# Kernel optimization log

Hardware: AMD Instinct MI355X
Metric: run time of the kernel (lower is better)

Reference implementation:

```python
import jax, jax.numpy as jnp
import numpy as np

EPS = 1e-5

@jax.custom_vjp
def ste_quantize(w):
    # abs-mean scale, round, clamp to {-1, 0, 1}
    scale = jnp.maximum(jnp.mean(jnp.abs(w)), EPS)
    return jnp.clip(jnp.round(w / scale), -1.0, 1.0)

def _ste_fwd(w):
    return ste_quantize(w), None

def _ste_bwd(_, g):
    # straight-through: gradient passes unchanged
    return (g,)

ste_quantize.defvjp(_ste_fwd, _ste_bwd)


def setup_inputs() -> dict:
    key = jax.random.key(0)
    k1, k2 = jax.random.split(key)
    x = jax.random.normal(k1, (8, 8192, 1024), dtype=jnp.float32)       # [B, S, in]
    weight = jax.random.normal(k2, (1024, 1024), dtype=jnp.float32) * 0.02  # [out, in]
    return {"x": x, "weight": weight}


def reference(x, weight):
    w_ternary = ste_quantize(weight)                         # [out, in] in {-1,0,1}
    scale = jnp.maximum(jnp.mean(jnp.abs(weight)), EPS)      # scalar (differentiable path)
    # F.linear(x, w_ternary * scale): out = x @ (w_ternary*scale)^T
    return jnp.einsum('bsi,oi->bso', x, w_ternary * scale)
```

## Files before the change

### kernel.cpp

```cpp
#include <hip/hip_runtime.h>
#include <stdint.h>

#define K_DIM 1024
#define N_DIM 1024

#define BM 256
#define BN 256
#define BK 32
#define NKT (K_DIM / BK)
#define NBUF 3
#define A_TILE (BM * BK)
#define B_TILE (BN * BK)

typedef __attribute__((ext_vector_type(8))) __bf16 bf16x8;
typedef __attribute__((ext_vector_type(4))) float f32x4;

__device__ __align__(16) unsigned short g_wq[N_DIM * K_DIM];
__device__ double g_partial[256];
__device__ float g_scale;

__device__ __forceinline__ unsigned int pack_bf16(float hi, float lo) {
  return __builtin_amdgcn_perm(__float_as_uint(hi), __float_as_uint(lo), 0x07060302u);
}

__global__ void absum_kernel(const float* __restrict__ w) {
  const int tid = threadIdx.x, bid = blockIdx.x;
  const float4* w4 = (const float4*)w;
  double s = 0.0;
#pragma unroll
  for (int i = 0; i < 4; i++) {
    float4 v = w4[bid * 1024 + i * 256 + tid];
    s += (double)fabsf(v.x) + (double)fabsf(v.y) + (double)fabsf(v.z) + (double)fabsf(v.w);
  }
#pragma unroll
  for (int o = 32; o > 0; o >>= 1) s += __shfl_down(s, o);
  __shared__ double sm[4];
  if ((tid & 63) == 0) sm[tid >> 6] = s;
  __syncthreads();
  if (tid == 0) g_partial[bid] = sm[0] + sm[1] + sm[2] + sm[3];
}

__global__ void scale_kernel() {
  const int tid = threadIdx.x;
  double v = g_partial[tid];
#pragma unroll
  for (int o = 32; o > 0; o >>= 1) v += __shfl_down(v, o);
  __shared__ double sm[4];
  if ((tid & 63) == 0) sm[tid >> 6] = v;
  __syncthreads();
  if (tid == 0) {
    double total = sm[0] + sm[1] + sm[2] + sm[3];
    double mean = total * (1.0 / 1048576.0);
    g_scale = (float)fmax(mean, 1e-5);
  }
}

__global__ void quant_kernel(const float* __restrict__ w) {
  const int idx = blockIdx.x * 256 + threadIdx.x;
  const float s = g_scale;
  float4 v = ((const float4*)w)[idx];
  float q0 = fminf(1.f, fmaxf(-1.f, rintf(v.x / s)));
  float q1 = fminf(1.f, fmaxf(-1.f, rintf(v.y / s)));
  float q2 = fminf(1.f, fmaxf(-1.f, rintf(v.z / s)));
  float q3 = fminf(1.f, fmaxf(-1.f, rintf(v.w / s)));
  ushort4 o;
  o.x = (unsigned short)(__float_as_uint(q0) >> 16);
  o.y = (unsigned short)(__float_as_uint(q1) >> 16);
  o.z = (unsigned short)(__float_as_uint(q2) >> 16);
  o.w = (unsigned short)(__float_as_uint(q3) >> 16);
  ((ushort4*)g_wq)[idx] = o;
}

__global__ __launch_bounds__(512, 2) void bitlinear_gemm(const float* __restrict__ x,
                                                         float* __restrict__ C) {
  __shared__ __align__(16) unsigned short As[NBUF * A_TILE];
  __shared__ __align__(16) unsigned short Bs[NBUF * B_TILE];

  const int tid  = threadIdx.x;
  const int lane = tid & 63;
  const int wave = tid >> 6;
  const int wm   = wave >> 2;
  const int wn   = wave & 3;
  const int lm   = lane & 15;
  const int lq   = lane >> 4;

  const int b       = blockIdx.x;
  const int cpx     = (int)(gridDim.x >> 3);
  const int logical = (b & 7) * cpx + (b >> 3);
  const int mt      = logical >> 2;
  const int nt      = logical & 3;
  const int m0      = mt * BM;
  const int n0      = nt * BN;

  f32x4 acc[8][4];
#pragma unroll
  for (int i = 0; i < 8; i++)
#pragma unroll
    for (int j = 0; j < 4; j++) acc[i][j] = (f32x4){0.f, 0.f, 0.f, 0.f};

  const int cswz = ((lane & 3) ^ ((lane >> 3) & 3)) * 8;
  const unsigned short* bSrc =
      g_wq + (size_t)(n0 + wave * 32 + (lane >> 2)) * K_DIM + cswz;
  const int ldsDst = wave * 32 * BK;

#define STAGE_B(tt, bb)                                                        \
  do {                                                                         \
    const unsigned short* s_ = bSrc + (tt) * BK;                               \
    unsigned short* d_ = &Bs[(bb) * B_TILE + ldsDst];                          \
    __builtin_amdgcn_global_load_lds(                                          \
        (const __attribute__((address_space(1))) unsigned int*)s_,             \
        (__attribute__((address_space(3))) unsigned int*)d_, 16, 0, 0);        \
    __builtin_amdgcn_global_load_lds(                                          \
        (const __attribute__((address_space(1))) unsigned int*)(s_ + 16 * K_DIM), \
        (__attribute__((address_space(3))) unsigned int*)(d_ + 16 * BK), 16, 0, 0); \
  } while (0)

  const int arow = wave * 32 + (lane >> 1);
  const int ah   = lane & 1;
  const int aswz = (lane >> 2) & 3;
  const float4* aGlb =
      (const float4*)(x + (size_t)(m0 + arow) * K_DIM + ah * 16);
  const int wo0 = arow * BK + (((2 * ah) ^ aswz) * 8);
  const int wo1 = arow * BK + (((2 * ah + 1) ^ aswz) * 8);

  float4 aR0, aR1, aR2, aR3;

#define LOAD_A(tt)                                                             \
  do {                                                                         \
    const float4* p_ = aGlb + (tt) * 8;                                        \
    aR0 = p_[0]; aR1 = p_[1]; aR2 = p_[2]; aR3 = p_[3];                        \
  } while (0)

#define CVT_WRITE_A(bb)                                                        \
  do {                                                                         \
    uint4 p0_, p1_;                                                            \
    p0_.x = pack_bf16(aR0.y, aR0.x); p0_.y = pack_bf16(aR0.w, aR0.z);          \
    p0_.z = pack_bf16(aR1.y, aR1.x); p0_.w = pack_bf16(aR1.w, aR1.z);          \
    p1_.x = pack_bf16(aR2.y, aR2.x); p1_.y = pack_bf16(aR2.w, aR2.z);          \
    p1_.z = pack_bf16(aR3.y, aR3.x); p1_.w = pack_bf16(aR3.w, aR3.z);          \
    *(uint4*)&As[(bb) * A_TILE + wo0] = p0_;                                   \
    *(uint4*)&As[(bb) * A_TILE + wo1] = p1_;                                   \
  } while (0)

  const int xorc = (((lm >> 1) & 3) ^ lq) * 8;
  const int aRd  = (wm * 128 + lm) * BK + xorc;
  const int bRd  = (wn * 64 + lm) * BK + xorc;

  {
    float4 t0, t1, t2, t3;
    {
      const float4* p_ = aGlb;
      t0 = p_[0]; t1 = p_[1]; t2 = p_[2]; t3 = p_[3];
    }
    STAGE_B(0, 0);
    LOAD_A(1);
    STAGE_B(1, 1);
    uint4 p0_, p1_;
    p0_.x = pack_bf16(t0.y, t0.x); p0_.y = pack_bf16(t0.w, t0.z);
    p0_.z = pack_bf16(t1.y, t1.x); p0_.w = pack_bf16(t1.w, t1.z);
    p1_.x = pack_bf16(t2.y, t2.x); p1_.y = pack_bf16(t2.w, t2.z);
    p1_.z = pack_bf16(t3.y, t3.x); p1_.w = pack_bf16(t3.w, t3.z);
    *(uint4*)&As[wo0] = p0_;
    *(uint4*)&As[wo1] = p1_;
  }
  asm volatile("s_waitcnt vmcnt(6) lgkmcnt(0)\n\ts_barrier" ::: "memory");

  int buf = 0;
#pragma unroll 1
  for (int t = 0; t < NKT; ++t) {
    const unsigned short* Ab = &As[buf * A_TILE + aRd];
    const unsigned short* Bb = &Bs[buf * B_TILE + bRd];
    const int nbuf = (buf + 2 >= NBUF) ? buf + 2 - NBUF : buf + 2;
    const int wbuf = (buf + 1 == NBUF) ? 0 : buf + 1;

    bf16x8 bfr[4], af[4];
#pragma unroll
    for (int nf = 0; nf < 4; ++nf) bfr[nf] = *(const bf16x8*)(Bb + nf * 16 * BK);
#pragma unroll
    for (int mf = 0; mf < 4; ++mf) af[mf] = *(const bf16x8*)(Ab + mf * 16 * BK);

    __builtin_amdgcn_s_setprio(1);
#pragma unroll
    for (int mf = 0; mf < 4; ++mf)
#pragma unroll
      for (int nf = 0; nf < 4; ++nf)
        acc[mf][nf] = __builtin_amdgcn_mfma_f32_16x16x32_bf16(af[mf], bfr[nf],
                                                              acc[mf][nf], 0, 0, 0);
    __builtin_amdgcn_s_setprio(0);

    bf16x8 af2[4];
#pragma unroll
    for (int mf = 0; mf < 4; ++mf)
      af2[mf] = *(const bf16x8*)(Ab + (mf + 4) * 16 * BK);

    if (t < NKT - 1) CVT_WRITE_A(wbuf);
    if (t < NKT - 2) {
      LOAD_A(t + 2);
      STAGE_B(t + 2, nbuf);
    }

    __builtin_amdgcn_s_setprio(1);
#pragma unroll
    for (int mf = 0; mf < 4; ++mf)
#pragma unroll
      for (int nf = 0; nf < 4; ++nf)
        acc[mf + 4][nf] = __builtin_amdgcn_mfma_f32_16x16x32_bf16(
            af2[mf], bfr[nf], acc[mf + 4][nf], 0, 0, 0);
    __builtin_amdgcn_s_setprio(0);

    if (t < NKT - 2)
      asm volatile("s_waitcnt vmcnt(6) lgkmcnt(0)\n\ts_barrier" ::: "memory");
    else if (t < NKT - 1)
      asm volatile("s_waitcnt vmcnt(0) lgkmcnt(0)\n\ts_barrier" ::: "memory");

    buf = wbuf;
  }
#undef STAGE_B
#undef LOAD_A
#undef CVT_WRITE_A

  const float s    = g_scale;
  const int   crow = m0 + wm * 128 + lq * 4;
  const int   ccol = n0 + wn * 64 + lm;
#pragma unroll
  for (int mf = 0; mf < 8; ++mf) {
#pragma unroll
    for (int nf = 0; nf < 4; ++nf) {
#pragma unroll
      for (int r = 0; r < 4; ++r) {
        C[(size_t)(crow + mf * 16 + r) * N_DIM + (ccol + nf * 16)] =
            acc[mf][nf][r] * s;
      }
    }
  }
}

extern "C" void kernel_launch(void* const* d_in, const int* in_sizes, int n_in,
                              void* d_out, int out_size, void* d_ws, size_t ws_size,
                              hipStream_t stream) {
  const float* x = (const float*)d_in[0];
  const float* w = (const float*)d_in[1];
  float* out = (float*)d_out;
  const int M = in_sizes[0] / K_DIM;

  hipLaunchKernelGGL(absum_kernel, dim3(256), dim3(256), 0, stream, w);
  hipLaunchKernelGGL(scale_kernel, dim3(1), dim3(256), 0, stream);
  hipLaunchKernelGGL(quant_kernel, dim3(1024), dim3(256), 0, stream, w);
  hipLaunchKernelGGL(bitlinear_gemm,
                     dim3((unsigned)(((size_t)M / BM) * (N_DIM / BN))),
                     dim3(512), 0, stream, x, out);
}
```

Before: 565.9 us.

## Shrink GEMM tiles to 128x128 with 4 waves and double buffering

Block tile drops from 256x256 with 8 waves to 128x128 with 4 waves. The triple-buffered, two-half MFMA pipeline becomes a simpler double-buffered loop that stages the next tile before one MFMA batch. The grid grows fourfold and launch bounds target more resident blocks per CU, aiming for better occupancy and latency hiding. In exchange, each x row tile is re-read and converted from fp32 to bf16 twice as often, and each block does fewer MFMAs per LDS byte.

```diff
diff --git a/kernel.cpp b/kernel.cpp
--- a/kernel.cpp
+++ b/kernel.cpp
@@ -4,11 +4,11 @@
 #define K_DIM 1024
 #define N_DIM 1024
 
-#define BM 256
-#define BN 256
+#define BM 128
+#define BN 128
 #define BK 32
 #define NKT (K_DIM / BK)
-#define NBUF 3
+#define NBUF 2
 #define A_TILE (BM * BK)
 #define B_TILE (BN * BK)
 
@@ -71,7 +71,7 @@
   ((ushort4*)g_wq)[idx] = o;
 }
 
-__global__ __launch_bounds__(512, 2) void bitlinear_gemm(const float* __restrict__ x,
+__global__ __launch_bounds__(256, 4) void bitlinear_gemm(const float* __restrict__ x,
                                                          float* __restrict__ C) {
   __shared__ __align__(16) unsigned short As[NBUF * A_TILE];
   __shared__ __align__(16) unsigned short Bs[NBUF * B_TILE];
@@ -79,22 +79,22 @@
   const int tid  = threadIdx.x;
   const int lane = tid & 63;
   const int wave = tid >> 6;
-  const int wm   = wave >> 2;
-  const int wn   = wave & 3;
+  const int wm   = (wave >> 1) * 64;
+  const int wn   = (wave & 1) * 64;
   const int lm   = lane & 15;
   const int lq   = lane >> 4;
 
   const int b       = blockIdx.x;
   const int cpx     = (int)(gridDim.x >> 3);
   const int logical = (b & 7) * cpx + (b >> 3);
-  const int mt      = logical >> 2;
-  const int nt      = logical & 3;
+  const int mt      = logical >> 3;
+  const int nt      = logical & 7;
   const int m0      = mt * BM;
   const int n0      = nt * BN;
 
-  f32x4 acc[8][4];
-#pragma unroll
-  for (int i = 0; i < 8; i++)
+  f32x4 acc[4][4];
+#pragma unroll
+  for (int i = 0; i < 4; i++)
 #pragma unroll
     for (int j = 0; j < 4; j++) acc[i][j] = (f32x4){0.f, 0.f, 0.f, 0.f};
 
@@ -115,9 +115,9 @@
         (__attribute__((address_space(3))) unsigned int*)(d_ + 16 * BK), 16, 0, 0); \
   } while (0)
 
-  const int arow = wave * 32 + (lane >> 1);
-  const int ah   = lane & 1;
-  const int aswz = (lane >> 2) & 3;
+  const int arow = tid >> 1;
+  const int ah   = tid & 1;
+  const int aswz = (tid >> 2) & 3;
   const float4* aGlb =
       (const float4*)(x + (size_t)(m0 + arow) * K_DIM + ah * 16);
   const int wo0 = arow * BK + (((2 * ah) ^ aswz) * 8);
@@ -143,41 +143,32 @@
   } while (0)
 
   const int xorc = (((lm >> 1) & 3) ^ lq) * 8;
-  const int aRd  = (wm * 128 + lm) * BK + xorc;
-  const int bRd  = (wn * 64 + lm) * BK + xorc;
-
-  {
-    float4 t0, t1, t2, t3;
-    {
-      const float4* p_ = aGlb;
-      t0 = p_[0]; t1 = p_[1]; t2 = p_[2]; t3 = p_[3];
-    }
-    STAGE_B(0, 0);
-    LOAD_A(1);
-    STAGE_B(1, 1);
-    uint4 p0_, p1_;
-    p0_.x = pack_bf16(t0.y, t0.x); p0_.y = pack_bf16(t0.w, t0.z);
-    p0_.z = pack_bf16(t1.y, t1.x); p0_.w = pack_bf16(t1.w, t1.z);
-    p1_.x = pack_bf16(t2.y, t2.x); p1_.y = pack_bf16(t2.w, t2.z);
-    p1_.z = pack_bf16(t3.y, t3.x); p1_.w = pack_bf16(t3.w, t3.z);
-    *(uint4*)&As[wo0] = p0_;
-    *(uint4*)&As[wo1] = p1_;
-  }
-  asm volatile("s_waitcnt vmcnt(6) lgkmcnt(0)\n\ts_barrier" ::: "memory");
+  const int aRd  = (wm + lm) * BK + xorc;
+  const int bRd  = (wn + lm) * BK + xorc;
+
+  LOAD_A(0);
+  STAGE_B(0, 0);
+  CVT_WRITE_A(0);
+  LOAD_A(1);
+  asm volatile("s_waitcnt vmcnt(4) lgkmcnt(0)\n\ts_barrier" ::: "memory");
 
   int buf = 0;
 #pragma unroll 1
   for (int t = 0; t < NKT; ++t) {
     const unsigned short* Ab = &As[buf * A_TILE + aRd];
     const unsigned short* Bb = &Bs[buf * B_TILE + bRd];
-    const int nbuf = (buf + 2 >= NBUF) ? buf + 2 - NBUF : buf + 2;
-    const int wbuf = (buf + 1 == NBUF) ? 0 : buf + 1;
 
     bf16x8 bfr[4], af[4];
 #pragma unroll
     for (int nf = 0; nf < 4; ++nf) bfr[nf] = *(const bf16x8*)(Bb + nf * 16 * BK);
 #pragma unroll
     for (int mf = 0; mf < 4; ++mf) af[mf] = *(const bf16x8*)(Ab + mf * 16 * BK);
+
+    if (t < NKT - 1) {
+      CVT_WRITE_A(buf ^ 1);
+      STAGE_B(t + 1, buf ^ 1);
+    }
+    if (t < NKT - 2) LOAD_A(t + 2);
 
     __builtin_amdgcn_s_setprio(1);
 #pragma unroll
@@ -188,42 +179,22 @@
                                                               acc[mf][nf], 0, 0, 0);
     __builtin_amdgcn_s_setprio(0);
 
-    bf16x8 af2[4];
-#pragma unroll
-    for (int mf = 0; mf < 4; ++mf)
-      af2[mf] = *(const bf16x8*)(Ab + (mf + 4) * 16 * BK);
-
-    if (t < NKT - 1) CVT_WRITE_A(wbuf);
-    if (t < NKT - 2) {
-      LOAD_A(t + 2);
-      STAGE_B(t + 2, nbuf);
-    }
-
-    __builtin_amdgcn_s_setprio(1);
-#pragma unroll
-    for (int mf = 0; mf < 4; ++mf)
-#pragma unroll
-      for (int nf = 0; nf < 4; ++nf)
-        acc[mf + 4][nf] = __builtin_amdgcn_mfma_f32_16x16x32_bf16(
-            af2[mf], bfr[nf], acc[mf + 4][nf], 0, 0, 0);
-    __builtin_amdgcn_s_setprio(0);
-
     if (t < NKT - 2)
-      asm volatile("s_waitcnt vmcnt(6) lgkmcnt(0)\n\ts_barrier" ::: "memory");
+      asm volatile("s_waitcnt vmcnt(4) lgkmcnt(0)\n\ts_barrier" ::: "memory");
     else if (t < NKT - 1)
       asm volatile("s_waitcnt vmcnt(0) lgkmcnt(0)\n\ts_barrier" ::: "memory");
 
-    buf = wbuf;
+    buf ^= 1;
   }
 #undef STAGE_B
 #undef LOAD_A
 #undef CVT_WRITE_A
 
   const float s    = g_scale;
-  const int   crow = m0 + wm * 128 + lq * 4;
-  const int   ccol = n0 + wn * 64 + lm;
-#pragma unroll
-  for (int mf = 0; mf < 8; ++mf) {
+  const int   crow = m0 + wm + lq * 4;
+  const int   ccol = n0 + wn + lm;
+#pragma unroll
+  for (int mf = 0; mf < 4; ++mf) {
 #pragma unroll
     for (int nf = 0; nf < 4; ++nf) {
 #pragma unroll
@@ -248,5 +219,5 @@
   hipLaunchKernelGGL(quant_kernel, dim3(1024), dim3(256), 0, stream, w);
   hipLaunchKernelGGL(bitlinear_gemm,
                      dim3((unsigned)(((size_t)M / BM) * (N_DIM / BN))),
-                     dim3(512), 0, stream, x, out);
-}
+                     dim3(256), 0, stream, x, out);
+}
```

Measured after the change: 648.6 us. 1.15x slower.
